# Optimization experiments

Measured on AMD Instinct MI355X. Metric: run time of the kernel, lower is better.

Reference implementation:

```python
import jax, jax.numpy as jnp
import numpy as np

NEAR = 0.1
FAR = 100.0


def quat_to_rotmat(q):
    q = q / jnp.linalg.norm(q, axis=-1, keepdims=True)
    w, x, y, z = q[..., 0], q[..., 1], q[..., 2], q[..., 3]
    R = jnp.stack([
        1 - 2 * (y * y + z * z), 2 * (x * y - z * w), 2 * (x * z + y * w),
        2 * (x * y + z * w), 1 - 2 * (x * x + z * z), 2 * (y * z - x * w),
        2 * (x * z - y * w), 2 * (y * z + x * w), 1 - 2 * (x * x + y * y)
    ], axis=-1)
    return R.reshape(q.shape[:-1] + (3, 3))


def _render_view(means, scales, rots, opac, sem, E, K3, H, W):
    # means [N,3] ego; E [4,4] ego2cam; K3 [3,3]
    means_cam = means @ E[:3, :3].T + E[:3, 3]  # [N,3]
    x_c, y_c, z = means_cam[:, 0], means_cam[:, 1], means_cam[:, 2]
    z_safe = jnp.maximum(z, 1e-4)
    fx, fy, cx, cy = K3[0, 0], K3[1, 1], K3[0, 2], K3[1, 2]
    u = x_c / z_safe * fx + cx
    v = y_c / z_safe * fy + cy
    # 3D covariance: Sigma = R diag(s)^2 R^T
    R = quat_to_rotmat(rots)              # [N,3,3]
    RS = R * scales[:, None, :]
    Sigma = RS @ jnp.swapaxes(RS, -1, -2)  # [N,3,3]
    Wc = E[:3, :3]
    Sigma_cam = jnp.einsum('ij,njk,lk->nil', Wc, Sigma, Wc)  # [N,3,3]
    # EWA Jacobian J [N,2,3]
    zero = jnp.zeros_like(z)
    J = jnp.stack([
        jnp.stack([fx / z_safe, zero, -fx * x_c / z_safe ** 2], axis=-1),
        jnp.stack([zero, fy / z_safe, -fy * y_c / z_safe ** 2], axis=-1),
    ], axis=-2)
    cov2d = jnp.einsum('nij,njk,nlk->nil', J, Sigma_cam, J)  # [N,2,2]
    a = jnp.maximum(cov2d[:, 0, 0], 0.3)
    c = jnp.maximum(cov2d[:, 1, 1], 0.3)
    bb = cov2d[:, 0, 1]
    det = a * c - bb * bb
    valid = (z > 0.01) & (det > 1e-8)
    det_s = jnp.where(det > 1e-8, det, 1.0)
    ia, ib, ic = c / det_s, -bb / det_s, a / det_s  # inverse 2x2 cov
    # per-pixel Mahalanobis distance, [N,H,W]
    px = jnp.arange(W, dtype=means.dtype)
    py = jnp.arange(H, dtype=means.dtype)
    dx = px[None, None, :] - u[:, None, None]   # [N,1,W]
    dy = py[None, :, None] - v[:, None, None]   # [N,H,1]
    d2 = (ia[:, None, None] * dx * dx + ic[:, None, None] * dy * dy
          + 2.0 * ib[:, None, None] * (dx * dy))
    g = jnp.exp(-0.5 * d2)
    visible = valid & (z > NEAR) & (u >= 0) & (u < W) & (v >= 0) & (v < H)
    alpha = jnp.where(visible[:, None, None],
                      jnp.clip(opac[:, None, None] * g, 0.0, 0.99), 0.0)
    # depth-sorted front-to-back alpha blending
    order = jnp.argsort(z)
    alpha_s = alpha[order]                                     # [N,H,W]
    feats = jnp.concatenate([sem, jnp.clip(z, NEAR, FAR)[:, None]], axis=-1)[order]  # [N,C+1]
    log1m = jnp.log1p(-alpha_s)
    T_excl = jnp.exp(jnp.cumsum(log1m, axis=0) - log1m)        # exclusive transmittance
    wgt = T_excl * alpha_s                                     # [N,H,W]
    rendered = jnp.einsum('nhw,nd->dhw', wgt, feats)           # [C+1,H,W]
    alpha_map = jnp.sum(wgt, axis=0)                           # [H,W]
    C = sem.shape[1]
    return rendered[C:C + 1], rendered[:C], alpha_map[None]


def reference(means, scales, rotations, opacities, semantic_features,
              target_intrinsics, target_cam2ego, H, W):
    ego2cam = jnp.linalg.inv(target_cam2ego)  # [B,M,4,4]
    B, M = target_cam2ego.shape[:2]
    deps, sems, alps = [], [], []
    for b in range(B):
        db, sb, ab = [], [], []
        for m in range(M):
            d, s, a = _render_view(means[b], scales[b], rotations[b],
                                   opacities[b, :, 0], semantic_features[b],
                                   ego2cam[b, m], target_intrinsics[b, m, :3, :3], H, W)
            db.append(d); sb.append(s); ab.append(a)
        deps.append(jnp.stack(db)); sems.append(jnp.stack(sb)); alps.append(jnp.stack(ab))
    depth_map = jnp.stack(deps)     # [B,M,1,H,W]
    semantic_map = jnp.stack(sems)  # [B,M,C,H,W]
    alpha_map = jnp.stack(alps)     # [B,M,1,H,W]
    return depth_map, semantic_map, alpha_map


def setup_inputs() -> dict:
    key = jax.random.key(0)
    ks = jax.random.split(key, 8)
    B, N, C, M, H, W = 1, 2048, 16, 2, 128, 128
    fx = fy = 128.0
    cx = cy = 64.0
    # gaussians inside the frustum: z in [2,40], |x|,|y| < 0.45*z
    z = jax.random.uniform(ks[0], (B, N), minval=2.0, maxval=40.0)
    x = z * jax.random.uniform(ks[1], (B, N), minval=-0.45, maxval=0.45)
    y = z * jax.random.uniform(ks[2], (B, N), minval=-0.45, maxval=0.45)
    means = jnp.stack([x, y, z], axis=-1).astype(jnp.float32)
    scales = jax.random.uniform(ks[3], (B, N, 3), minval=0.05, maxval=0.5).astype(jnp.float32)
    rotations = jax.random.normal(ks[4], (B, N, 4), dtype=jnp.float32)
    opacities = jax.random.uniform(ks[5], (B, N, 1), minval=0.05, maxval=0.95).astype(jnp.float32)
    semantic_features = jax.random.normal(ks[6], (B, N, C), dtype=jnp.float32)
    K = jnp.array([[fx, 0, cx, 0], [0, fy, cy, 0], [0, 0, 1, 0], [0, 0, 0, 1]], dtype=jnp.float32)
    target_intrinsics = jnp.broadcast_to(K, (B, M, 4, 4))
    c2e0 = jnp.eye(4, dtype=jnp.float32)
    c2e1 = c2e0.at[0, 3].set(0.5)
    target_cam2ego = jnp.broadcast_to(jnp.stack([c2e0, c2e1]), (B, M, 4, 4))
    return {"means": means, "scales": scales, "rotations": rotations,
            "opacities": opacities, "semantic_features": semantic_features,
            "target_intrinsics": target_intrinsics, "target_cam2ego": target_cam2ego,
            "H": H, "W": W}
```

## Files before the change

### kernel.cpp

```cpp
#include <hip/hip_runtime.h>
#include <cmath>


#define MAXC   16
#define MAXBM  8
#define NSEG   16
#define RTPB   (NSEG * 64)
#define ROWS1  9
#define ROWS2  10
#define INVIS_KEY 0x7FFFFFFF

__device__ void inv4x4_rows3(const float* __restrict__ src, float* __restrict__ Eout) {
    double m[16];
#pragma unroll
    for (int j = 0; j < 16; ++j) m[j] = (double)src[j];
    double inv[16];
    inv[0]  =  m[5]*m[10]*m[15] - m[5]*m[11]*m[14] - m[9]*m[6]*m[15] + m[9]*m[7]*m[14] + m[13]*m[6]*m[11] - m[13]*m[7]*m[10];
    inv[4]  = -m[4]*m[10]*m[15] + m[4]*m[11]*m[14] + m[8]*m[6]*m[15] - m[8]*m[7]*m[14] - m[12]*m[6]*m[11] + m[12]*m[7]*m[10];
    inv[8]  =  m[4]*m[9]*m[15]  - m[4]*m[11]*m[13] - m[8]*m[5]*m[15] + m[8]*m[7]*m[13] + m[12]*m[5]*m[11] - m[12]*m[7]*m[9];
    inv[12] = -m[4]*m[9]*m[14]  + m[4]*m[10]*m[13] + m[8]*m[5]*m[14] - m[8]*m[6]*m[13] - m[12]*m[5]*m[10] + m[12]*m[6]*m[9];
    inv[1]  = -m[1]*m[10]*m[15] + m[1]*m[11]*m[14] + m[9]*m[2]*m[15] - m[9]*m[3]*m[14] - m[13]*m[2]*m[11] + m[13]*m[3]*m[10];
    inv[5]  =  m[0]*m[10]*m[15] - m[0]*m[11]*m[14] - m[8]*m[2]*m[15] + m[8]*m[3]*m[14] + m[12]*m[2]*m[11] - m[12]*m[3]*m[10];
    inv[9]  = -m[0]*m[9]*m[15]  + m[0]*m[11]*m[13] + m[8]*m[1]*m[15] - m[8]*m[3]*m[13] - m[12]*m[1]*m[11] + m[12]*m[3]*m[9];
    inv[13] =  m[0]*m[9]*m[14]  - m[0]*m[10]*m[13] - m[8]*m[1]*m[14] + m[8]*m[2]*m[13] + m[12]*m[1]*m[10] - m[12]*m[2]*m[9];
    inv[2]  =  m[1]*m[6]*m[15]  - m[1]*m[7]*m[14]  - m[5]*m[2]*m[15] + m[5]*m[3]*m[14] + m[13]*m[2]*m[7]  - m[13]*m[3]*m[6];
    inv[6]  = -m[0]*m[6]*m[15]  + m[0]*m[7]*m[14]  + m[4]*m[2]*m[15] - m[4]*m[3]*m[14] - m[12]*m[2]*m[7]  + m[12]*m[3]*m[6];
    inv[10] =  m[0]*m[5]*m[15]  - m[0]*m[7]*m[13]  - m[4]*m[1]*m[15] + m[4]*m[3]*m[13] + m[12]*m[1]*m[7]  - m[12]*m[3]*m[5];
    inv[14] = -m[0]*m[5]*m[14]  + m[0]*m[6]*m[13]  + m[4]*m[1]*m[14] - m[4]*m[2]*m[13] - m[12]*m[1]*m[6]  + m[12]*m[2]*m[5];
    inv[3]  = -m[1]*m[6]*m[11]  + m[1]*m[7]*m[10]  + m[5]*m[2]*m[11] - m[5]*m[3]*m[10] - m[9]*m[2]*m[7]   + m[9]*m[3]*m[6];
    inv[7]  =  m[0]*m[6]*m[11]  - m[0]*m[7]*m[10]  - m[4]*m[2]*m[11] + m[4]*m[3]*m[10] + m[8]*m[2]*m[7]   - m[8]*m[3]*m[6];
    inv[11] = -m[0]*m[5]*m[11]  + m[0]*m[7]*m[9]   + m[4]*m[1]*m[11] - m[4]*m[3]*m[9]  - m[8]*m[1]*m[7]   + m[8]*m[3]*m[5];
    inv[15] =  m[0]*m[5]*m[10]  - m[0]*m[6]*m[9]   - m[4]*m[1]*m[10] + m[4]*m[2]*m[9]  + m[8]*m[1]*m[6]   - m[8]*m[2]*m[5];
    double det = m[0]*inv[0] + m[1]*inv[4] + m[2]*inv[8] + m[3]*inv[12];
    double rdet = 1.0 / det;
#pragma unroll
    for (int r = 0; r < 3; ++r)
#pragma unroll
        for (int c = 0; c < 4; ++c)
            Eout[r * 4 + c] = (float)(inv[r * 4 + c] * rdet);
}

__global__ __launch_bounds__(256) void preprocess_kernel(
    const float* __restrict__ means, const float* __restrict__ scales,
    const float* __restrict__ rots,  const float* __restrict__ intr,
    const float* __restrict__ cam2ego,
    int* __restrict__ ikey, float* __restrict__ uu, float* __restrict__ vv,
    float* __restrict__ cia, float* __restrict__ cib, float* __restrict__ cic,
    float* __restrict__ cex, float* __restrict__ cey,
    float* __restrict__ crbc, float* __restrict__ crba,
    int B, int M, int N, int W, int H)
{
    __shared__ float Esh[MAXBM * 12];
    int BM = B * M;
    if (threadIdx.x < (unsigned)BM)
        inv4x4_rows3(cam2ego + (size_t)threadIdx.x * 16, Esh + threadIdx.x * 12);
    __syncthreads();

    int gid = blockIdx.x * 256 + threadIdx.x;
    if (gid >= BM * N) return;
    int bm = gid / N;
    int n  = gid - bm * N;
    int b  = bm / M;
    const float* Ep = Esh + bm * 12;
    const float* mp = means + ((size_t)b * N + n) * 3;
    float mx = mp[0], my = mp[1], mz = mp[2];
    float x_c = Ep[0]*mx + Ep[1]*my + Ep[2]*mz  + Ep[3];
    float y_c = Ep[4]*mx + Ep[5]*my + Ep[6]*mz  + Ep[7];
    float z   = Ep[8]*mx + Ep[9]*my + Ep[10]*mz + Ep[11];
    const float* K = intr + (size_t)bm * 16;
    float fx = K[0], fy = K[5], cx = K[2], cy = K[6];
    float zs = fmaxf(z, 1e-4f);
    float u = x_c / zs * fx + cx;
    float v = y_c / zs * fy + cy;
    const float* qp = rots + ((size_t)b * N + n) * 4;
    float qw = qp[0], qx = qp[1], qy = qp[2], qz = qp[3];
    float qn = sqrtf(qw*qw + qx*qx + qy*qy + qz*qz);
    qw /= qn; qx /= qn; qy /= qn; qz /= qn;
    float R00 = 1.f - 2.f*(qy*qy + qz*qz), R01 = 2.f*(qx*qy - qz*qw), R02 = 2.f*(qx*qz + qy*qw);
    float R10 = 2.f*(qx*qy + qz*qw), R11 = 1.f - 2.f*(qx*qx + qz*qz), R12 = 2.f*(qy*qz - qx*qw);
    float R20 = 2.f*(qx*qz - qy*qw), R21 = 2.f*(qy*qz + qx*qw), R22 = 1.f - 2.f*(qx*qx + qy*qy);
    const float* sp = scales + ((size_t)b * N + n) * 3;
    float s0 = sp[0]*sp[0], s1 = sp[1]*sp[1], s2 = sp[2]*sp[2];
    float S00 = R00*R00*s0 + R01*R01*s1 + R02*R02*s2;
    float S01 = R00*R10*s0 + R01*R11*s1 + R02*R12*s2;
    float S02 = R00*R20*s0 + R01*R21*s1 + R02*R22*s2;
    float S11 = R10*R10*s0 + R11*R11*s1 + R12*R12*s2;
    float S12 = R10*R20*s0 + R11*R21*s1 + R12*R22*s2;
    float S22 = R20*R20*s0 + R21*R21*s1 + R22*R22*s2;
    float W00 = Ep[0], W01 = Ep[1], W02 = Ep[2];
    float W10 = Ep[4], W11 = Ep[5], W12 = Ep[6];
    float W20 = Ep[8], W21 = Ep[9], W22 = Ep[10];
    float A00 = W00*S00 + W01*S01 + W02*S02;
    float A01 = W00*S01 + W01*S11 + W02*S12;
    float A02 = W00*S02 + W01*S12 + W02*S22;
    float A10 = W10*S00 + W11*S01 + W12*S02;
    float A11 = W10*S01 + W11*S11 + W12*S12;
    float A12 = W10*S02 + W11*S12 + W12*S22;
    float A20 = W20*S00 + W21*S01 + W22*S02;
    float A21 = W20*S01 + W21*S11 + W22*S12;
    float A22 = W20*S02 + W21*S12 + W22*S22;
    float Sc00 = A00*W00 + A01*W01 + A02*W02;
    float Sc01 = A00*W10 + A01*W11 + A02*W12;
    float Sc02 = A00*W20 + A01*W21 + A02*W22;
    float Sc11 = A10*W10 + A11*W11 + A12*W12;
    float Sc12 = A10*W20 + A11*W21 + A12*W22;
    float Sc22 = A20*W20 + A21*W21 + A22*W22;
    float j00 = fx / zs,  j02 = -fx * x_c / (zs * zs);
    float j11 = fy / zs,  j12 = -fy * y_c / (zs * zs);
    float c00 = j00*j00*Sc00 + 2.f*j00*j02*Sc02 + j02*j02*Sc22;
    float c01 = j00*(Sc01*j11 + Sc02*j12) + j02*(Sc12*j11 + Sc22*j12);
    float c11 = j11*j11*Sc11 + 2.f*j11*j12*Sc12 + j12*j12*Sc22;
    float a  = fmaxf(c00, 0.3f);
    float cc = fmaxf(c11, 0.3f);
    float bb = c01;
    float det = a * cc - bb * bb;
    bool valid = (z > 0.01f) && (det > 1e-8f);
    float det_s = (det > 1e-8f) ? det : 1.0f;
    float ia = cc / det_s, ib = -bb / det_s, ic = a / det_s;
    uu[gid] = u;  vv[gid] = v;
    cia[gid] = ia;  cib[gid] = ib;  cic[gid] = ic;
    cex[gid] = sqrtf(34.0f * a);
    cey[gid] = sqrtf(34.0f * cc);
    crbc[gid] = -bb / a;
    crba[gid] = -bb / cc;
    bool visible = valid && (z > 0.1f) &&
                   (u >= 0.f) && (u < (float)W) && (v >= 0.f) && (v < (float)H);
    ikey[gid] = visible ? __float_as_int(z) : INVIS_KEY;
}

__global__ __launch_bounds__(64) void rankpack_kernel(
    const int* __restrict__ ikey,
    const float* __restrict__ uu, const float* __restrict__ vv,
    const float* __restrict__ cia, const float* __restrict__ cib,
    const float* __restrict__ cic, const float* __restrict__ cex,
    const float* __restrict__ cey, const float* __restrict__ crbc,
    const float* __restrict__ crba,
    const float* __restrict__ opac, const float* __restrict__ sem,
    float4* __restrict__ pk0, float4* __restrict__ pk1,
    float4* __restrict__ pk2,
    float* __restrict__ psem, int* __restrict__ pcount,
    int B, int M, int N, int C)
{
    int lane  = threadIdx.x & 63;
    int nch64 = (N + 63) >> 6;
    int chunk = blockIdx.x;
    int bm = chunk / nch64;
    int cl = chunk - bm * nch64;
    int i  = (cl << 6) + lane;
    const int* kb = ikey + (size_t)bm * N;
    int ki  = (i < N) ? kb[i] : INVIS_KEY;
    int kip = ki + 1;
    int rank = 0, tot = 0;
    int kj = (lane < N) ? kb[lane] : INVIS_KEY;
    for (int jc = 0; jc < nch64; ++jc) {
        int kcur = kj;
        if (jc + 1 < nch64) {
            int jn = ((jc + 1) << 6) + lane;
            kj = (jn < N) ? kb[jn] : INVIS_KEY;
        }
        tot += (int)__popcll(__ballot(kcur != INVIS_KEY));
        if (jc < cl) {
#pragma unroll
            for (int gg = 0; gg < 64; ++gg)
                rank += (__builtin_amdgcn_readlane(kcur, gg) < kip);
        } else if (jc > cl) {
#pragma unroll
            for (int gg = 0; gg < 64; ++gg)
                rank += (__builtin_amdgcn_readlane(kcur, gg) < ki);
        } else {
#pragma unroll
            for (int gg = 0; gg < 64; ++gg) {
                int kk = (gg < lane) ? kip : ki;
                rank += (__builtin_amdgcn_readlane(kcur, gg) < kk);
            }
        }
    }
    if (cl == 0 && lane == 0) pcount[bm] = tot;
    if (i < N && ki != INVIS_KEY) {
        int b = bm / M;
        size_t src = (size_t)bm * N + i;
        size_t dst = (size_t)bm * N + rank;
        float z = __int_as_float(ki);
        pk0[dst] = make_float4(uu[src], vv[src], cex[src], cey[src]);
        pk1[dst] = make_float4(cia[src], cib[src], cic[src],
                               opac[(size_t)b * N + i]);
        pk2[dst] = make_float4(fminf(fmaxf(z, 0.1f), 100.0f),
                               crbc[src], crba[src], 0.f);
        const float* spc = sem + ((size_t)b * N + i) * C;
        float* dpc = psem + dst * C;
        int c4 = C & ~3;
        for (int q = 0; q < c4; q += 4)
            *(float4*)(dpc + q) = *(const float4*)(spc + q);
        for (int q = c4; q < C; ++q) dpc[q] = spc[q];
    }
}

__global__ __launch_bounds__(RTPB) void raster_kernel(
    const float4* __restrict__ pk0, const float4* __restrict__ pk1,
    const float4* __restrict__ pk2,
    const float* __restrict__ psem, const int* __restrict__ pcount,
    float* __restrict__ out,
    int BM, int N, int C, int H, int W, int ntx, int nty)
{
    __shared__ float comb[NSEG * ROWS2 * 64];
    int wave = threadIdx.x >> 6;
    int lane = threadIdx.x & 63;
    int tile = blockIdx.x;
    int tpv = ntx * nty;
    int bm  = tile / tpv;
    int rem = tile - bm * tpv;
    int tyi = rem / ntx;
    int txi = rem - tyi * ntx;
    int lx = lane & 7, ly = lane >> 3;
    float fxp = (float)(txi * 8 + lx), fyp = (float)(tyi * 8 + ly);
    float x0 = (float)(txi * 8),     y0 = (float)(tyi * 8);
    float x1 = (float)(txi * 8 + 7), y1 = (float)(tyi * 8 + 7);

    int cnt = pcount[bm];
    int seg = (cnt + NSEG - 1) / NSEG;
    int gs = wave * seg;
    int ge = min(gs + seg, cnt);

    float T = 1.0f, accA = 0.f, accD = 0.f;
    float accS[MAXC];
#pragma unroll
    for (int q = 0; q < MAXC; ++q) accS[q] = 0.f;

    for (int base = gs; base < ge; base += 64) {
        if (!__any(T >= 1e-6f)) break;
        int g = base + lane;
        bool inr = g < ge;
        int gc = inr ? g : (ge - 1);
        size_t src = (size_t)bm * N + gc;
        float4 P0 = pk0[src];
        float4 P1 = pk1[src];
        float4 P2 = pk2[src];
        float dx0 = x0 - P0.x, dx1 = x1 - P0.x;
        float dy0 = y0 - P0.y, dy1 = y1 - P0.y;
        bool aabb = (dx0 <= P0.z) && (-dx1 <= P0.z) &&
                    (dy0 <= P0.w) && (-dy1 <= P0.w);
        bool inside = (dx0 <= 0.f) && (dx1 >= 0.f) && (dy0 <= 0.f) && (dy1 >= 0.f);
        float t, q0, q1, q2, q3;
        t  = fminf(fmaxf(P2.y * dx0, dy0), dy1);
        q0 = P1.x * dx0 * dx0 + t * (P1.z * t + 2.f * P1.y * dx0);
        t  = fminf(fmaxf(P2.y * dx1, dy0), dy1);
        q1 = P1.x * dx1 * dx1 + t * (P1.z * t + 2.f * P1.y * dx1);
        t  = fminf(fmaxf(P2.z * dy0, dx0), dx1);
        q2 = P1.z * dy0 * dy0 + t * (P1.x * t + 2.f * P1.y * dy0);
        t  = fminf(fmaxf(P2.z * dy1, dx0), dx1);
        q3 = P1.z * dy1 * dy1 + t * (P1.x * t + 2.f * P1.y * dy1);
        float mind2 = inside ? 0.f : fminf(fminf(q0, q1), fminf(q2, q3));
        unsigned long long mask = __ballot(inr && aabb && (mind2 <= 34.0f));
        if (!mask) continue;

        size_t sb = (size_t)bm * N + base;
        int su = __builtin_amdgcn_readfirstlane(__ffsll((long long)mask) - 1);
        mask &= mask - 1;
        float4 Q0 = pk0[sb + su];
        float4 Q1 = pk1[sb + su];
        float4 Q2 = pk2[sb + su];
        const float4* sv = (const float4*)(psem + (sb + su) * MAXC);
        float4 c0 = sv[0], c1 = sv[1], c2 = sv[2], c3 = sv[3];
        for (;;) {
            bool more = (mask != 0ull);
            int sn = more ? (__ffsll((long long)mask) - 1) : 0;
            mask &= mask - 1;
            sn = __builtin_amdgcn_readfirstlane(sn);
            float4 nQ0 = pk0[sb + sn];
            float4 nQ1 = pk1[sb + sn];
            float4 nQ2 = pk2[sb + sn];
            const float4* nsv = (const float4*)(psem + (sb + sn) * MAXC);
            float4 n0 = nsv[0], n1 = nsv[1], n2 = nsv[2], n3 = nsv[3];
            float dx = fxp - Q0.x, dy = fyp - Q0.y;
            float d2 = Q1.x*dx*dx + Q1.z*dy*dy + 2.0f*Q1.y*(dx*dy);
            float gvl = __expf(-0.5f * d2);
            float alpha = fminf(Q1.w * gvl, 0.99f);
            float w = T * alpha;
            T -= w;
            accD += w * Q2.x;
            accA += w;
            accS[0]  += w * c0.x;  accS[1]  += w * c0.y;
            accS[2]  += w * c0.z;  accS[3]  += w * c0.w;
            accS[4]  += w * c1.x;  accS[5]  += w * c1.y;
            accS[6]  += w * c1.z;  accS[7]  += w * c1.w;
            accS[8]  += w * c2.x;  accS[9]  += w * c2.y;
            accS[10] += w * c2.z;  accS[11] += w * c2.w;
            accS[12] += w * c3.x;  accS[13] += w * c3.y;
            accS[14] += w * c3.z;  accS[15] += w * c3.w;
            if (!more) break;
            Q0 = nQ0; Q1 = nQ1; Q2 = nQ2;
            c0 = n0; c1 = n1; c2 = n2; c3 = n3;
        }
    }

    int px = lane;
    int pxx = txi * 8 + (px & 7);
    int pyy = tyi * 8 + (px >> 3);
    bool inb = (pxx < W) && (pyy < H);
    size_t HW  = (size_t)H * W;
    size_t pix = (size_t)pyy * W + pxx;
    size_t BMHW = (size_t)BM * HW;

    float* my = comb + (wave * ROWS1) * 64 + lane;
    my[0 * 64] = T;
    my[1 * 64] = accD;
    my[2 * 64] = accA;
#pragma unroll
    for (int k = 0; k < 6; ++k) my[(3 + k) * 64] = accS[k];
    __syncthreads();

    float pre[NSEG];
    pre[0] = 1.f;
#pragma unroll
    for (int w = 1; w < NSEG; ++w)
        pre[w] = pre[w-1] * comb[((w-1) * ROWS1) * 64 + px];

    if (wave < 8) {
        int row, outc;
        if (wave == 0)      { row = 1;        outc = 0; }
        else if (wave <= 6) { row = 2 + wave; outc = wave; }
        else                { row = 2;        outc = C + 1; }
        float val = 0.f;
#pragma unroll
        for (int w = 0; w < NSEG; ++w)
            val += pre[w] * comb[(w * ROWS1 + row) * 64 + px];
        if (inb) {
            float* dst;
            if (outc == 0)      dst = out + (size_t)bm * HW + pix;
            else if (outc <= C) dst = out + BMHW + (size_t)bm * C * HW + (size_t)(outc-1) * HW + pix;
            else                dst = out + BMHW + BMHW * C + (size_t)bm * HW + pix;
            *dst = val;
        }
    }
    __syncthreads();

    float* my2 = comb + (wave * ROWS2) * 64 + lane;
#pragma unroll
    for (int k = 0; k < 10; ++k) my2[k * 64] = accS[6 + k];
    __syncthreads();

    if (wave < 10) {
        int k = wave;
        float val = 0.f;
#pragma unroll
        for (int w = 0; w < NSEG; ++w)
            val += pre[w] * comb[(w * ROWS2 + k) * 64 + px];
        if (inb) {
            int outc = 7 + k;
            float* dst = out + BMHW + (size_t)bm * C * HW + (size_t)(outc-1) * HW + pix;
            *dst = val;
        }
    }
}

extern "C" void kernel_launch(void* const* d_in, const int* in_sizes, int n_in,
                              void* d_out, int out_size, void* d_ws, size_t ws_size,
                              hipStream_t stream) {
    const float* means  = (const float*)d_in[0];
    const float* scales = (const float*)d_in[1];
    const float* rots   = (const float*)d_in[2];
    const float* opac   = (const float*)d_in[3];
    const float* sem    = (const float*)d_in[4];
    const float* intr   = (const float*)d_in[5];
    const float* c2e    = (const float*)d_in[6];
    float* out = (float*)d_out;

    int B  = 1;
    int BM = in_sizes[6] / 16;
    int M  = BM / B;
    int N  = in_sizes[0] / (3 * B);
    int C  = in_sizes[4] / (B * N);
    long HWl = (long)out_size / ((long)BM * (C + 2));
    int H = (int)(sqrt((double)HWl) + 0.5);
    int W = (int)(HWl / H);
    int ntx = (W + 7) / 8, nty = (H + 7) / 8;
    int ntiles = ntx * nty * BM;
    int nch64  = (N + 63) >> 6;

    float* ws = (float*)d_ws;
    size_t off = 0;
    size_t BMN  = (size_t)BM * N;
    int*   ikey = (int*)(ws + off); off += BMN;
    float* uu   = ws + off; off += BMN;
    float* vv   = ws + off; off += BMN;
    float* cia  = ws + off; off += BMN;
    float* cib  = ws + off; off += BMN;
    float* cic  = ws + off; off += BMN;
    float* cex  = ws + off; off += BMN;
    float* cey  = ws + off; off += BMN;
    float* crbc = ws + off; off += BMN;
    float* crba = ws + off; off += BMN;
    off = (off + 3) & ~(size_t)3;
    float4* pk0 = (float4*)(ws + off); off += BMN * 4;
    float4* pk1 = (float4*)(ws + off); off += BMN * 4;
    float4* pk2 = (float4*)(ws + off); off += BMN * 4;
    float* psem = ws + off; off += BMN * C;
    int* pcount = (int*)(ws + off); off += BM;

    int tot = BM * N;
    preprocess_kernel<<<(tot + 255) / 256, 256, 0, stream>>>(
        means, scales, rots, intr, c2e,
        ikey, uu, vv, cia, cib, cic, cex, cey, crbc, crba, B, M, N, W, H);

    rankpack_kernel<<<BM * nch64, 64, 0, stream>>>(
        ikey, uu, vv, cia, cib, cic, cex, cey, crbc, crba, opac, sem,
        pk0, pk1, pk2, psem, pcount, B, M, N, C);

    raster_kernel<<<ntiles, RTPB, 0, stream>>>(
        pk0, pk1, pk2, psem, pcount, out, BM, N, C, H, W, ntx, nty);
}
```

Measured before the change: 139.5 us.

## Add per-tile binning pass and broadcast gaussian data via readlane in raster

```diff
diff --git a/kernel.cpp b/kernel.cpp
--- a/kernel.cpp
+++ b/kernel.cpp
@@ -6,9 +6,16 @@
 #define MAXBM  8
 #define NSEG   16
 #define RTPB   (NSEG * 64)
+#define BINW   8
+#define BINT   (BINW * 64)
+#define MAXSEG 256
 #define ROWS1  9
 #define ROWS2  10
 #define INVIS_KEY 0x7FFFFFFF
+
+__device__ __forceinline__ float rlf(float x, int l) {
+    return __int_as_float(__builtin_amdgcn_readlane(__float_as_int(x), l));
+}
 
 __device__ void inv4x4_rows3(const float* __restrict__ src, float* __restrict__ Eout) {
     double m[16];
@@ -195,14 +202,14 @@
     }
 }
 
-__global__ __launch_bounds__(RTPB) void raster_kernel(
+__global__ __launch_bounds__(BINT) void binlist_kernel(
     const float4* __restrict__ pk0, const float4* __restrict__ pk1,
-    const float4* __restrict__ pk2,
-    const float* __restrict__ psem, const int* __restrict__ pcount,
-    float* __restrict__ out,
-    int BM, int N, int C, int H, int W, int ntx, int nty)
+    const float4* __restrict__ pk2, const int* __restrict__ pcount,
+    int* __restrict__ list, int* __restrict__ tilecount,
+    int BM, int N, int ntx, int nty)
 {
-    __shared__ float comb[NSEG * ROWS2 * 64];
+    __shared__ int stage[BINW][MAXSEG];
+    __shared__ int wcnt[BINW];
     int wave = threadIdx.x >> 6;
     int lane = threadIdx.x & 63;
     int tile = blockIdx.x;
@@ -211,23 +218,16 @@
     int rem = tile - bm * tpv;
     int tyi = rem / ntx;
     int txi = rem - tyi * ntx;
-    int lx = lane & 7, ly = lane >> 3;
-    float fxp = (float)(txi * 8 + lx), fyp = (float)(tyi * 8 + ly);
     float x0 = (float)(txi * 8),     y0 = (float)(tyi * 8);
     float x1 = (float)(txi * 8 + 7), y1 = (float)(tyi * 8 + 7);
 
     int cnt = pcount[bm];
-    int seg = (cnt + NSEG - 1) / NSEG;
+    int seg = (cnt + BINW - 1) / BINW;
     int gs = wave * seg;
     int ge = min(gs + seg, cnt);
 
-    float T = 1.0f, accA = 0.f, accD = 0.f;
-    float accS[MAXC];
-#pragma unroll
-    for (int q = 0; q < MAXC; ++q) accS[q] = 0.f;
-
+    int nlocal = 0;
     for (int base = gs; base < ge; base += 64) {
-        if (!__any(T >= 1e-6f)) break;
         int g = base + lane;
         bool inr = g < ge;
         int gc = inr ? g : (ge - 1);
@@ -251,45 +251,86 @@
         q3 = P1.z * dy1 * dy1 + t * (P1.x * t + 2.f * P1.y * dy1);
         float mind2 = inside ? 0.f : fminf(fminf(q0, q1), fminf(q2, q3));
         unsigned long long mask = __ballot(inr && aabb && (mind2 <= 34.0f));
-        if (!mask) continue;
-
-        size_t sb = (size_t)bm * N + base;
-        int su = __builtin_amdgcn_readfirstlane(__ffsll((long long)mask) - 1);
-        mask &= mask - 1;
-        float4 Q0 = pk0[sb + su];
-        float4 Q1 = pk1[sb + su];
-        float4 Q2 = pk2[sb + su];
-        const float4* sv = (const float4*)(psem + (sb + su) * MAXC);
-        float4 c0 = sv[0], c1 = sv[1], c2 = sv[2], c3 = sv[3];
-        for (;;) {
-            bool more = (mask != 0ull);
-            int sn = more ? (__ffsll((long long)mask) - 1) : 0;
-            mask &= mask - 1;
-            sn = __builtin_amdgcn_readfirstlane(sn);
-            float4 nQ0 = pk0[sb + sn];
-            float4 nQ1 = pk1[sb + sn];
-            float4 nQ2 = pk2[sb + sn];
-            const float4* nsv = (const float4*)(psem + (sb + sn) * MAXC);
-            float4 n0 = nsv[0], n1 = nsv[1], n2 = nsv[2], n3 = nsv[3];
-            float dx = fxp - Q0.x, dy = fyp - Q0.y;
-            float d2 = Q1.x*dx*dx + Q1.z*dy*dy + 2.0f*Q1.y*(dx*dy);
+        if ((mask >> lane) & 1ull) {
+            int pos = nlocal + (int)__popcll(mask & ((1ull << lane) - 1ull));
+            stage[wave][pos] = g;
+        }
+        nlocal += (int)__popcll(mask);
+    }
+    if (lane == 0) wcnt[wave] = nlocal;
+    __syncthreads();
+    int offs = 0, total = 0;
+    for (int w = 0; w < BINW; ++w) {
+        if (w < wave) offs += wcnt[w];
+        total += wcnt[w];
+    }
+    int* dst = list + (size_t)tile * N;
+    for (int i = lane; i < nlocal; i += 64) dst[offs + i] = stage[wave][i];
+    if (threadIdx.x == 0) tilecount[tile] = total;
+}
+
+__global__ __launch_bounds__(RTPB) void raster_kernel(
+    const float4* __restrict__ pk0, const float4* __restrict__ pk1,
+    const float4* __restrict__ pk2,
+    const float* __restrict__ psem,
+    const int* __restrict__ list, const int* __restrict__ tilecount,
+    float* __restrict__ out,
+    int BM, int N, int C, int H, int W, int ntx, int nty)
+{
+    __shared__ float comb[NSEG * ROWS2 * 64];
+    int wave = threadIdx.x >> 6;
+    int lane = threadIdx.x & 63;
+    int tile = blockIdx.x;
+    int tpv = ntx * nty;
+    int bm  = tile / tpv;
+    int rem = tile - bm * tpv;
+    int tyi = rem / ntx;
+    int txi = rem - tyi * ntx;
+    int lx = lane & 7, ly = lane >> 3;
+    float fxp = (float)(txi * 8 + lx), fyp = (float)(tyi * 8 + ly);
+
+    int cnt = tilecount[tile];
+    int seg = (cnt + NSEG - 1) / NSEG;
+    int gs = wave * seg;
+    int ge = min(gs + seg, cnt);
+
+    float T = 1.0f, accA = 0.f, accD = 0.f;
+    float accS[MAXC];
+#pragma unroll
+    for (int q = 0; q < MAXC; ++q) accS[q] = 0.f;
+
+    const int* tl = list + (size_t)tile * N;
+    for (int base = gs; base < ge; base += 64) {
+        int g = base + lane;
+        bool inr = g < ge;
+        int idx = tl[inr ? g : (ge - 1)];
+        size_t src = (size_t)bm * N + idx;
+        float4 P0 = pk0[src];
+        float4 P1 = pk1[src];
+        float4 P2 = pk2[src];
+        float sf[MAXC];
+        {
+            const float4* spc = (const float4*)(psem + src * MAXC);
+#pragma unroll
+            for (int q = 0; q < MAXC / 4; ++q) {
+                float4 f = spc[q];
+                sf[q*4+0] = f.x; sf[q*4+1] = f.y; sf[q*4+2] = f.z; sf[q*4+3] = f.w;
+            }
+        }
+        int nev = min(64, ge - base);
+        for (int gg = 0; gg < nev; ++gg) {
+            float u  = rlf(P0.x, gg), v  = rlf(P0.y, gg);
+            float ia = rlf(P1.x, gg), ib = rlf(P1.y, gg), ic = rlf(P1.z, gg);
+            float dx = fxp - u, dy = fyp - v;
+            float d2 = ia*dx*dx + ic*dy*dy + 2.0f*ib*(dx*dy);
             float gvl = __expf(-0.5f * d2);
-            float alpha = fminf(Q1.w * gvl, 0.99f);
+            float alpha = fminf(rlf(P1.w, gg) * gvl, 0.99f);
             float w = T * alpha;
             T -= w;
-            accD += w * Q2.x;
+            accD += w * rlf(P2.x, gg);
             accA += w;
-            accS[0]  += w * c0.x;  accS[1]  += w * c0.y;
-            accS[2]  += w * c0.z;  accS[3]  += w * c0.w;
-            accS[4]  += w * c1.x;  accS[5]  += w * c1.y;
-            accS[6]  += w * c1.z;  accS[7]  += w * c1.w;
-            accS[8]  += w * c2.x;  accS[9]  += w * c2.y;
-            accS[10] += w * c2.z;  accS[11] += w * c2.w;
-            accS[12] += w * c3.x;  accS[13] += w * c3.y;
-            accS[14] += w * c3.z;  accS[15] += w * c3.w;
-            if (!more) break;
-            Q0 = nQ0; Q1 = nQ1; Q2 = nQ2;
-            c0 = n0; c1 = n1; c2 = n2; c3 = n3;
+#pragma unroll
+            for (int ch = 0; ch < MAXC; ++ch) accS[ch] += w * rlf(sf[ch], gg);
         }
     }
 
@@ -396,6 +437,8 @@
     float4* pk2 = (float4*)(ws + off); off += BMN * 4;
     float* psem = ws + off; off += BMN * C;
     int* pcount = (int*)(ws + off); off += BM;
+    int* list   = (int*)(ws + off); off += (size_t)ntiles * N;
+    int* tcnt   = (int*)(ws + off); off += ntiles;
 
     int tot = BM * N;
     preprocess_kernel<<<(tot + 255) / 256, 256, 0, stream>>>(
@@ -406,6 +449,9 @@
         ikey, uu, vv, cia, cib, cic, cex, cey, crbc, crba, opac, sem,
         pk0, pk1, pk2, psem, pcount, B, M, N, C);
 
+    binlist_kernel<<<ntiles, BINT, 0, stream>>>(
+        pk0, pk1, pk2, pcount, list, tcnt, BM, N, ntx, nty);
+
     raster_kernel<<<ntiles, RTPB, 0, stream>>>(
-        pk0, pk1, pk2, psem, pcount, out, BM, N, C, H, W, ntx, nty);
-}
+        pk0, pk1, pk2, psem, list, tcnt, out, BM, N, C, H, W, ntx, nty);
+}
```

After: 121.2 us. 13.1% less time.
